# Kernel optimization log

Hardware: AMD Instinct MI355X
Metric: run time of the kernel (lower is better)

Reference implementation:

```python
import jax, jax.numpy as jnp
import numpy as np

N_NODES = 50000
N_EDGES = 300000
D = 256          # in_dim = out_dim (residual)
DE = 256         # edge relation dim
K = 2            # num_kgs
H = 4            # heads
L = 2            # layers
DH = D // H


def _routed_linear(x, W, b, idx):
    # x:[E,din], W:[K,din,dout], b:[K,dout], idx:[E] in [0,K)
    # Compute all K branches (K is tiny) then select per edge.
    outs = jnp.einsum('ed,kdo->keo', x, W) + b[:, None, :]
    return outs[idx, jnp.arange(idx.shape[0])]


def _layernorm(x, g, b):
    mu = jnp.mean(x, axis=-1, keepdims=True)
    var = jnp.mean(jnp.square(x - mu), axis=-1, keepdims=True)
    return (x - mu) * jax.lax.rsqrt(var + 1e-5) * g + b


def _mga_layer(h, src, dst, kg_src, kg_dst, beta, rel,
               ln_g, ln_b, Wt, bt, Wq, bq, Wk, bk):
    N = h.shape[0]
    E = src.shape[0]
    residual = h
    hn = _layernorm(h, ln_g, ln_b)
    x_j = hn[src]                       # [E,D] gathered source feats
    x_i = hn[dst]                       # [E,D] gathered target feats
    # per-edge KG-routed transfer of concatenated (x_j, relation emb)
    xj_t = jax.nn.gelu(_routed_linear(jnp.concatenate([x_j, rel], axis=1), Wt, bt, kg_src),
                       approximate=False)
    q = _routed_linear(x_i, Wq, bq, kg_dst).reshape(E, H, DH)
    k = _routed_linear(xj_t, Wk, bk, kg_src).reshape(E, H, DH)
    # per-edge multi-head dot product, scaled by edge_beta_r then 1/sqrt(dh)
    att = jnp.sum(q * k, axis=-1) * beta[:, None] / jnp.sqrt(jnp.asarray(DH, h.dtype))  # [E,H]
    # scatter-softmax over incoming edges of each target node
    m = jax.ops.segment_max(att, dst, num_segments=N)          # [N,H]
    e = jnp.exp(att - m[dst])
    denom = jax.ops.segment_sum(e, dst, num_segments=N)        # [N,H]
    a = e / (denom[dst] + 1e-16)                                # [E,H]
    msg = (a[:, :, None] * xj_t.reshape(E, H, DH)).reshape(E, D)
    aggr = jax.ops.segment_sum(msg, dst, num_segments=N)        # [N,D]
    return residual + jax.nn.gelu(aggr, approximate=False)


def setup_inputs() -> dict:
    key = jax.random.key(0)
    ks = jax.random.split(key, 10)
    x = jax.random.normal(ks[0], (N_NODES, D), dtype=jnp.float32)
    edge_index = jax.random.randint(ks[1], (2, N_EDGES), 0, N_NODES, dtype=jnp.int32)
    edge_kg_index = jax.random.randint(ks[2], (2, N_EDGES), 0, K, dtype=jnp.int32)
    edge_beta_r = jax.random.uniform(ks[3], (N_EDGES,), dtype=jnp.float32)
    edge_rel_emb = jax.random.normal(ks[4], (N_EDGES, DE), dtype=jnp.float32)
    return {
        'x': x,
        'edge_index': edge_index,
        'edge_kg_index': edge_kg_index,
        'edge_beta_r': edge_beta_r,
        'edge_rel_emb': edge_rel_emb,
        'ln_g': jnp.ones((L, D), jnp.float32),
        'ln_b': jnp.zeros((L, D), jnp.float32),
        'Wt': jax.random.normal(ks[5], (L, K, D + DE, D), jnp.float32) / np.sqrt(D + DE),
        'bt': jnp.zeros((L, K, D), jnp.float32),
        'Wq': jax.random.normal(ks[6], (L, K, D, D), jnp.float32) / np.sqrt(D),
        'bq': jnp.zeros((L, K, D), jnp.float32),
        'Wk': jax.random.normal(ks[7], (L, K, D, D), jnp.float32) / np.sqrt(D),
        'bk': jnp.zeros((L, K, D), jnp.float32),
    }


def reference(x, edge_index, edge_kg_index, edge_beta_r, edge_rel_emb,
              ln_g, ln_b, Wt, bt, Wq, bq, Wk, bk):
    src, dst = edge_index[0], edge_index[1]          # j (source), i (target)
    kg_src, kg_dst = edge_kg_index[0], edge_kg_index[1]
    h = x  # dropout is identity in eval mode
    for l in range(L):
        h = _mga_layer(h, src, dst, kg_src, kg_dst, edge_beta_r, edge_rel_emb,
                       ln_g[l], ln_b[l], Wt[l], bt[l], Wq[l], bq[l], Wk[l], bk[l])
    return h
```

## Files before the change

kernel.cpp:

```cpp
#include <hip/hip_runtime.h>
#include <hip/hip_bf16.h>

#define NN 50000
#define NE 300000
#define DD 256
#define NCHUNK 293

typedef __hip_bfloat16 bf16;
typedef __attribute__((ext_vector_type(8))) short bf16x8;
typedef __attribute__((ext_vector_type(4))) float f32x4;

__device__ __forceinline__ float bf2f(bf16 v) { return __bfloat162float(v); }
__device__ __forceinline__ unsigned short f2b(float v) {
    bf16 t = __float2bfloat16(v);
    return *reinterpret_cast<unsigned short*>(&t);
}
__device__ __forceinline__ float b2f_bits(unsigned short u) {
    return __uint_as_float(((unsigned)u) << 16);
}
__device__ __forceinline__ float gelu_f(float v) {
    return 0.5f * v * (1.f + erff(v * 0.70710678118654752f));
}
__device__ __forceinline__ void gl2lds16(const uint4* g, uint4* l) {
    __builtin_amdgcn_global_load_lds(
        (const __attribute__((address_space(1))) void*)g,
        (__attribute__((address_space(3))) void*)l, 16, 0, 0);
}

__global__ void part_count(const int* __restrict__ kg, int* __restrict__ bcnt) {
    int base = blockIdx.x * 1024;
    __shared__ int wc[4];
    int t = threadIdx.x, wave = t >> 6, lane = t & 63;
    int cnt = 0;
    #pragma unroll
    for (int s = 0; s < 4; ++s) {
        int j = base + s * 256 + t;
        int is0 = (j < NE && kg[j] == 0) ? 1 : 0;
        unsigned long long m = __ballot(is0);
        if (lane == 0) cnt += __popcll(m);
    }
    if (lane == 0) wc[wave] = cnt;
    __syncthreads();
    if (t == 0) bcnt[blockIdx.x] = wc[0] + wc[1] + wc[2] + wc[3];
}

__global__ void part_scan(const int* __restrict__ bcnt, int* __restrict__ bofs,
                          int* __restrict__ meta, int n) {
    if (threadIdx.x == 0 && blockIdx.x == 0) {
        int run = 0;
        for (int i = 0; i < n; ++i) { bofs[i] = run; run += bcnt[i]; }
        meta[0] = run;
    }
}

__global__ void part_scatter(const int* __restrict__ kg, const int* __restrict__ bofs,
                             const int* __restrict__ meta, int* __restrict__ perm) {
    int base = blockIdx.x * 1024;
    int c0 = meta[0];
    __shared__ int wz[4];
    int t = threadIdx.x, wave = t >> 6, lane = t & 63;
    int zrun = bofs[blockIdx.x];
    for (int s = 0; s < 4; ++s) {
        int j = base + s * 256 + t;
        int valid = j < NE;
        int is0 = (valid && kg[j] == 0) ? 1 : 0;
        unsigned long long m = __ballot(is0);
        int zb = __popcll(m & ((1ull << lane) - 1ull));
        if (lane == 0) wz[wave] = __popcll(m);
        __syncthreads();
        int wbefore = 0;
        for (int w = 0; w < wave; ++w) wbefore += wz[w];
        int zeros_before = zrun + wbefore + zb;
        if (valid) {
            int pos = is0 ? zeros_before : (c0 + (j - zeros_before));
            perm[pos] = j;
        }
        int stepz = wz[0] + wz[1] + wz[2] + wz[3];
        __syncthreads();
        zrun += stepz;
    }
}

__global__ void deg_hist(const int* __restrict__ dst, int* __restrict__ deg) {
    int i = blockIdx.x * blockDim.x + threadIdx.x;
    if (i < NE) atomicAdd(&deg[dst[i]], 1);
}

__global__ __launch_bounds__(1024) void scan_nodes(const int* __restrict__ deg,
                                                   int* __restrict__ ofs) {
    __shared__ int pex[1025];
    int t = threadIdx.x;
    const int C = (NN + 1023) / 1024;
    int base = t * C;
    int s = 0;
    for (int j = 0; j < C; ++j) { int idx = base + j; if (idx < NN) s += deg[idx]; }
    pex[t + 1] = s;
    __syncthreads();
    if (t == 0) {
        pex[0] = 0;
        for (int i = 1; i <= 1024; ++i) pex[i] += pex[i - 1];
    }
    __syncthreads();
    int run = pex[t];
    for (int j = 0; j < C; ++j) {
        int idx = base + j;
        if (idx < NN) { ofs[idx] = run; run += deg[idx]; }
    }
    if (t == 1023) ofs[NN] = pex[1024];
}

__global__ void copy_int(const int* __restrict__ a, int* __restrict__ b, int n) {
    int i = blockIdx.x * blockDim.x + threadIdx.x;
    if (i < n) b[i] = a[i];
}

__global__ void csr_fill(const int* __restrict__ dst, int* __restrict__ cur,
                         int* __restrict__ eid) {
    int i = blockIdx.x * blockDim.x + threadIdx.x;
    if (i < NE) {
        int p = atomicAdd(&cur[dst[i]], 1);
        eid[p] = i;
    }
}

__global__ void cast_x_kernel(const float* __restrict__ x, float* __restrict__ h, int n4) {
    for (int i = blockIdx.x * blockDim.x + threadIdx.x; i < n4; i += gridDim.x * blockDim.x)
        ((float4*)h)[i] = ((const float4*)x)[i];
}

__global__ void f2b_vec_kernel(const float* __restrict__ in, ushort* __restrict__ out, long n4) {
    long i0 = (long)blockIdx.x * blockDim.x + threadIdx.x;
    long stride = (long)gridDim.x * blockDim.x;
    for (long i = i0; i < n4; i += stride) {
        float4 v = ((const float4*)in)[i];
        ushort4 o;
        o.x = f2b(v.x); o.y = f2b(v.y); o.z = f2b(v.z); o.w = f2b(v.w);
        ((ushort4*)out)[i] = o;
    }
}

__global__ void transpose_w_kernel(const float* __restrict__ in, ushort* __restrict__ out,
                                   int shift, long total) {
    long i0 = (long)blockIdx.x * blockDim.x + threadIdx.x;
    long stride = (long)gridDim.x * blockDim.x;
    long dmask = ((long)1 << shift) - 1;
    for (long i = i0; i < total; i += stride) {
        long d = i & dmask;
        long rest = i >> shift;
        long o = rest & 255;
        long s = rest >> 8;
        out[i] = f2b(in[((s << shift) + d) * 256 + o]);
    }
}

__global__ void fill_kernel(float* __restrict__ p, float v, int n) {
    for (int i = blockIdx.x * blockDim.x + threadIdx.x; i < n; i += gridDim.x * blockDim.x)
        p[i] = v;
}

__global__ __launch_bounds__(256) void ln_kernel(const float* __restrict__ h,
        const float* __restrict__ g, const float* __restrict__ b, bf16* __restrict__ hn) {
    int n = blockIdx.x * 4 + (threadIdx.x >> 6);
    if (n >= NN) return;
    int t = threadIdx.x & 63;
    float4 v = ((const float4*)(h + (size_t)n * DD))[t];
    float s  = v.x + v.y + v.z + v.w;
    float s2 = v.x * v.x + v.y * v.y + v.z * v.z + v.w * v.w;
    #pragma unroll
    for (int off = 32; off; off >>= 1) {
        s  += __shfl_down(s, off);
        s2 += __shfl_down(s2, off);
    }
    s = __shfl(s, 0); s2 = __shfl(s2, 0);
    float mu  = s * (1.f / DD);
    float var = s2 * (1.f / DD) - mu * mu;
    float rs  = rsqrtf(var + 1e-5f);
    float vv[4] = {v.x, v.y, v.z, v.w};
    ushort4 pk;
    unsigned short* pku = (unsigned short*)&pk;
    #pragma unroll
    for (int j = 0; j < 4; ++j) {
        int c = t * 4 + j;
        pku[j] = f2b((vv[j] - mu) * rs * g[c] + b[c]);
    }
    ((ushort4*)(hn + (size_t)n * DD))[t] = pk;
}

__global__ __launch_bounds__(512) void qn_mfma(
        const bf16* __restrict__ hn, const ushort* __restrict__ WqT,
        const float* __restrict__ bq, ushort* __restrict__ qn) {
    __shared__ uint4 xh[64 * 32];
    __shared__ float bqs[2][256];
    int t = threadIdx.x;
    int n0 = blockIdx.x * 64;
    int wave = t >> 6, lane = t & 63;
    if (t < 256) { bqs[0][t] = bq[t]; bqs[1][t] = bq[256 + t]; }
    const uint4* hn4 = (const uint4*)hn;
    #pragma unroll
    for (int j = 0; j < 4; ++j) {
        int pr = wave * 4 + j;
        int r2 = pr * 2 + (lane >> 5);
        int node = n0 + r2; if (node >= NN) node = NN - 1;
        int s = lane & 31;
        gl2lds16(hn4 + (size_t)node * 32 + (s ^ (r2 & 7)), &xh[pr * 64]);
    }
    __syncthreads();
    int lr = lane & 15, lg = lane >> 4;
    f32x4 acc[2][2][4];
    #pragma unroll
    for (int b = 0; b < 2; ++b)
        #pragma unroll
        for (int m = 0; m < 2; ++m)
            #pragma unroll
            for (int n = 0; n < 4; ++n) acc[b][m][n] = (f32x4){0.f, 0.f, 0.f, 0.f};
    const char* xhb = (const char*)xh;
    const ushort* qr0 = WqT + (size_t)(wave * 32 + lr) * 256 + lg * 8;
    const ushort* qr1 = WqT + (size_t)(wave * 32 + 16 + lr) * 256 + lg * 8;
    #pragma unroll
    for (int kk = 0; kk < 8; ++kk) {
        bf16x8 a00 = *(const bf16x8*)(qr0 + kk * 32);
        bf16x8 a01 = *(const bf16x8*)(qr1 + kk * 32);
        bf16x8 a10 = *(const bf16x8*)(qr0 + 65536 + kk * 32);
        bf16x8 a11 = *(const bf16x8*)(qr1 + 65536 + kk * 32);
        bf16x8 bfr[4];
        #pragma unroll
        for (int n = 0; n < 4; ++n) {
            int r = n * 16 + lr;
            bfr[n] = *(const bf16x8*)(xhb + r * 512 + (((kk * 4 + lg) ^ (r & 7)) << 4));
        }
        #pragma unroll
        for (int n = 0; n < 4; ++n) {
            acc[0][0][n] = __builtin_amdgcn_mfma_f32_16x16x32_bf16(a00, bfr[n], acc[0][0][n], 0, 0, 0);
            acc[0][1][n] = __builtin_amdgcn_mfma_f32_16x16x32_bf16(a01, bfr[n], acc[0][1][n], 0, 0, 0);
            acc[1][0][n] = __builtin_amdgcn_mfma_f32_16x16x32_bf16(a10, bfr[n], acc[1][0][n], 0, 0, 0);
            acc[1][1][n] = __builtin_amdgcn_mfma_f32_16x16x32_bf16(a11, bfr[n], acc[1][1][n], 0, 0, 0);
        }
    }
    #pragma unroll
    for (int n = 0; n < 4; ++n) {
        int e = n * 16 + lr;
        int node = n0 + e;
        if (node < NN) {
            #pragma unroll
            for (int br = 0; br < 2; ++br)
                #pragma unroll
                for (int m = 0; m < 2; ++m) {
                    int ob = wave * 32 + m * 16 + lg * 4;
                    f32x4 a = acc[br][m][n];
                    ushort4 pk;
                    unsigned short* pu = (unsigned short*)&pk;
                    #pragma unroll
                    for (int r = 0; r < 4; ++r) pu[r] = f2b(a[r] + bqs[br][ob + r]);
                    *(ushort4*)(qn + ((size_t)br * NN + node) * 256 + ob) = pk;
                }
        }
    }
}

template<int RELB>
__global__ __launch_bounds__(512, 4) void transfer_mfma(
        const bf16* __restrict__ hn, const float* __restrict__ rel,
        const ushort* __restrict__ relb,
        const int* __restrict__ src, const int* __restrict__ dst,
        const int* __restrict__ kgd,
        const int* __restrict__ perm, const int* __restrict__ meta,
        const ushort* __restrict__ WtT, const float* __restrict__ bt,
        const ushort* __restrict__ WkT, const float* __restrict__ bk,
        const ushort* __restrict__ qn, const float* __restrict__ beta,
        bf16* __restrict__ xjt, float* __restrict__ att) {
    __shared__ uint4 xh[64 * 32];
    __shared__ float bts[256], bks[256];
    __shared__ float patt[8][64];
    __shared__ int sge[64], ssrc[64], sdst[64], sgd[64], sval[64];
    int t = threadIdx.x;
    int c0 = meta[0];
    int tiles0 = (c0 + 63) >> 6;
    int tiles1 = (NE - c0 + 63) >> 6;
    int bid = blockIdx.x;
    if (bid >= tiles0 + tiles1) return;
    int kgt, start, end;
    if (bid < tiles0) { kgt = 0; start = bid * 64; end = c0; }
    else              { kgt = 1; start = c0 + (bid - tiles0) * 64; end = NE; }
    int wave = t >> 6, lane = t & 63;
    if (t < 64) {
        int pos = start + t;
        int v = pos < end;
        int ge = perm[v ? pos : end - 1];
        sge[t] = ge; sval[t] = v; ssrc[t] = src[ge]; sdst[t] = dst[ge]; sgd[t] = kgd[ge];
    } else if (t >= 256) {
        int c = t & 255;
        bts[c] = bt[kgt * 256 + c];
        bks[c] = bk[kgt * 256 + c];
    }
    __syncthreads();
    const uint4* hn4 = (const uint4*)hn;
    #pragma unroll
    for (int j = 0; j < 4; ++j) {
        int pr = wave * 4 + j;
        int r2 = pr * 2 + (lane >> 5);
        int s = lane & 31;
        gl2lds16(hn4 + (size_t)ssrc[r2] * 32 + (s ^ (r2 & 7)), &xh[pr * 64]);
    }
    __syncthreads();
    int lr = lane & 15, lg = lane >> 4;
    f32x4 acc[2][4];
    #pragma unroll
    for (int m = 0; m < 2; ++m)
        #pragma unroll
        for (int n = 0; n < 4; ++n) acc[m][n] = (f32x4){0.f, 0.f, 0.f, 0.f};
    const char* xhb = (const char*)xh;
    const ushort* wb = WtT + (size_t)kgt * 131072;
    const ushort* wrow0 = wb + (size_t)(wave * 32 + lr) * 512 + lg * 8;
    const ushort* wrow1 = wb + (size_t)(wave * 32 + 16 + lr) * 512 + lg * 8;
    #pragma unroll
    for (int kk = 0; kk < 8; ++kk) {
        bf16x8 a0 = *(const bf16x8*)(wrow0 + kk * 32);
        bf16x8 a1 = *(const bf16x8*)(wrow1 + kk * 32);
        bf16x8 bfr[4];
        #pragma unroll
        for (int n = 0; n < 4; ++n) {
            int r = n * 16 + lr;
            bfr[n] = *(const bf16x8*)(xhb + r * 512 + (((kk * 4 + lg) ^ (r & 7)) << 4));
        }
        #pragma unroll
        for (int m = 0; m < 2; ++m)
            #pragma unroll
            for (int n = 0; n < 4; ++n)
                acc[m][n] = __builtin_amdgcn_mfma_f32_16x16x32_bf16((m ? a1 : a0), bfr[n], acc[m][n], 0, 0, 0);
    }
    __syncthreads();
    if (RELB) {
        const uint4* rb4 = (const uint4*)relb;
        #pragma unroll
        for (int j = 0; j < 4; ++j) {
            int pr = wave * 4 + j;
            int r2 = pr * 2 + (lane >> 5);
            int s = lane & 31;
            gl2lds16(rb4 + (size_t)sge[r2] * 32 + (s ^ (r2 & 7)), &xh[pr * 64]);
        }
    } else {
        #pragma unroll
        for (int i = 0; i < 8; ++i) {
            int r = i * 8 + wave;
            float4 f = ((const float4*)(rel + (size_t)sge[r] * 256))[lane];
            ushort4 o;
            o.x = f2b(f.x); o.y = f2b(f.y); o.z = f2b(f.z); o.w = f2b(f.w);
            int s = lane >> 1;
            char* bp = (char*)&xh[r * 32] + (((s ^ (r & 7)) << 4) | ((lane & 1) << 3));
            *(ushort4*)bp = o;
        }
    }
    __syncthreads();
    #pragma unroll
    for (int kk = 8; kk < 16; ++kk) {
        bf16x8 a0 = *(const bf16x8*)(wrow0 + kk * 32);
        bf16x8 a1 = *(const bf16x8*)(wrow1 + kk * 32);
        int ks = (kk & 7) * 4 + lg;
        bf16x8 bfr[4];
        #pragma unroll
        for (int n = 0; n < 4; ++n) {
            int r = n * 16 + lr;
            bfr[n] = *(const bf16x8*)(xhb + r * 512 + ((ks ^ (r & 7)) << 4));
        }
        #pragma unroll
        for (int m = 0; m < 2; ++m)
            #pragma unroll
            for (int n = 0; n < 4; ++n)
                acc[m][n] = __builtin_amdgcn_mfma_f32_16x16x32_bf16((m ? a1 : a0), bfr[n], acc[m][n], 0, 0, 0);
    }
    __syncthreads();
    char* xob = (char*)xh;
    #pragma unroll
    for (int n = 0; n < 4; ++n) {
        int e = n * 16 + lr;
        #pragma unroll
        for (int m = 0; m < 2; ++m) {
            int ob = wave * 32 + m * 16 + lg * 4;
            f32x4 a = acc[m][n];
            ushort4 pk;
            unsigned short* pu = (unsigned short*)&pk;
            #pragma unroll
            for (int r = 0; r < 4; ++r)
                pu[r] = f2b(gelu_f(a[r] + bts[ob + r]));
            int bofs = ob * 2;
            int slot = ((bofs >> 4) ^ (e & 7));
            *(ushort4*)(xob + e * 512 + slot * 16 + (bofs & 15)) = pk;
        }
    }
    __syncthreads();
    #pragma unroll
    for (int m = 0; m < 2; ++m)
        #pragma unroll
        for (int n = 0; n < 4; ++n) acc[m][n] = (f32x4){0.f, 0.f, 0.f, 0.f};
    const ushort* kbw = WkT + (size_t)kgt * 65536;
    const ushort* kr0 = kbw + (size_t)(wave * 32 + lr) * 256 + lg * 8;
    const ushort* kr1 = kbw + (size_t)(wave * 32 + 16 + lr) * 256 + lg * 8;
    #pragma unroll
    for (int kk = 0; kk < 8; ++kk) {
        bf16x8 a0 = *(const bf16x8*)(kr0 + kk * 32);
        bf16x8 a1 = *(const bf16x8*)(kr1 + kk * 32);
        bf16x8 bfr[4];
        #pragma unroll
        for (int n = 0; n < 4; ++n) {
            int r = n * 16 + lr;
            bfr[n] = *(const bf16x8*)(xob + r * 512 + (((kk * 4 + lg) ^ (r & 7)) << 4));
        }
        #pragma unroll
        for (int n = 0; n < 4; ++n) {
            acc[0][n] = __builtin_amdgcn_mfma_f32_16x16x32_bf16(a0, bfr[n], acc[0][n], 0, 0, 0);
            acc[1][n] = __builtin_amdgcn_mfma_f32_16x16x32_bf16(a1, bfr[n], acc[1][n], 0, 0, 0);
        }
    }
    float p[4];
    #pragma unroll
    for (int n = 0; n < 4; ++n) {
        int e = n * 16 + lr;
        size_t qb = ((size_t)sgd[e] * NN + sdst[e]) * 256;
        float s = 0.f;
        #pragma unroll
        for (int m = 0; m < 2; ++m) {
            int ob = wave * 32 + m * 16 + lg * 4;
            ushort4 qv = *(const ushort4*)(qn + qb + ob);
            f32x4 kcv = acc[m][n];
            s = fmaf(b2f_bits(qv.x), kcv[0] + bks[ob + 0], s);
            s = fmaf(b2f_bits(qv.y), kcv[1] + bks[ob + 1], s);
            s = fmaf(b2f_bits(qv.z), kcv[2] + bks[ob + 2], s);
            s = fmaf(b2f_bits(qv.w), kcv[3] + bks[ob + 3], s);
        }
        p[n] = s;
    }
    #pragma unroll
    for (int n = 0; n < 4; ++n) {
        p[n] += __shfl_xor(p[n], 16);
        p[n] += __shfl_xor(p[n], 32);
    }
    if (lane < 16) {
        #pragma unroll
        for (int n = 0; n < 4; ++n) patt[wave][n * 16 + lr] = p[n];
    }
    uint4* xjv = (uint4*)xjt;
    #pragma unroll
    for (int i = 0; i < 4; ++i) {
        int flat = i * 512 + t;
        int r = flat >> 5, c = flat & 31;
        if (sval[r])
            xjv[(size_t)sge[r] * 32 + c] = *(const uint4*)(xob + r * 512 + ((c ^ (r & 7)) << 4));
    }
    __syncthreads();
    if (t < 256) {
        int e = t & 63, h = t >> 6;
        if (sval[e]) {
            int ge = sge[e];
            att[(size_t)ge * 4 + h] = (patt[2 * h][e] + patt[2 * h + 1][e]) * beta[ge] * 0.125f;
        }
    }
}

__global__ __launch_bounds__(256) void aggregate_kernel(
        const float* __restrict__ att, const bf16* __restrict__ xjt,
        const int* __restrict__ eid, const int* __restrict__ ofs,
        float* __restrict__ h) {
    int node = blockIdx.x * 4 + (threadIdx.x >> 6);
    if (node >= NN) return;
    int lane = threadIdx.x & 63;
    int hh = lane >> 4;
    int beg = ofs[node], end = ofs[node + 1];
    float m = -1e30f;
    for (int i = beg; i < end; ++i)
        m = fmaxf(m, att[(size_t)eid[i] * 4 + hh]);
    float den = 0.f;
    float a0 = 0.f, a1 = 0.f, a2 = 0.f, a3 = 0.f;
    for (int i = beg; i < end; ++i) {
        int e = eid[i];
        float wgt = expf(att[(size_t)e * 4 + hh] - m);
        den += wgt;
        ushort4 v = *(const ushort4*)((const ushort*)xjt + (size_t)e * 256 + lane * 4);
        a0 = fmaf(wgt, b2f_bits(v.x), a0);
        a1 = fmaf(wgt, b2f_bits(v.y), a1);
        a2 = fmaf(wgt, b2f_bits(v.z), a2);
        a3 = fmaf(wgt, b2f_bits(v.w), a3);
    }
    float inv = 1.f / (den + 1e-16f);
    float4 hv = ((float4*)(h + (size_t)node * 256))[lane];
    hv.x += gelu_f(a0 * inv);
    hv.y += gelu_f(a1 * inv);
    hv.z += gelu_f(a2 * inv);
    hv.w += gelu_f(a3 * inv);
    ((float4*)(h + (size_t)node * 256))[lane] = hv;
}

extern "C" void kernel_launch(void* const* d_in, const int* in_sizes, int n_in,
                              void* d_out, int out_size, void* d_ws, size_t ws_size,
                              hipStream_t stream) {
    const float* x    = (const float*)d_in[0];
    const int*   ei   = (const int*)d_in[1];
    const int*   ekg  = (const int*)d_in[2];
    const float* beta = (const float*)d_in[3];
    const float* rel  = (const float*)d_in[4];
    const float* ln_g = (const float*)d_in[5];
    const float* ln_b = (const float*)d_in[6];
    const float* Wt   = (const float*)d_in[7];
    const float* bt   = (const float*)d_in[8];
    const float* Wq   = (const float*)d_in[9];
    const float* bq   = (const float*)d_in[10];
    const float* Wk   = (const float*)d_in[11];
    const float* bk   = (const float*)d_in[12];

    float* h = (float*)d_out;

    const int* srcp = ei;
    const int* dstp = ei + NE;
    const int* kgs  = ekg;
    const int* kgd  = ekg + NE;

    char* w = (char*)d_ws;
    float*  att   = (float*)w;  w += (size_t)NE * 4 * 4;
    bf16*   hn    = (bf16*)w;   w += (size_t)NN * DD * 2;
    bf16*   xjt   = (bf16*)w;   w += (size_t)NE * DD * 2;
    ushort* qn    = (ushort*)w; w += (size_t)2 * NN * DD * 2;
    ushort* WtT   = (ushort*)w; w += (size_t)4 * 256 * 512 * 2;
    ushort* WqT   = (ushort*)w; w += (size_t)4 * 256 * 256 * 2;
    ushort* WkT   = (ushort*)w; w += (size_t)4 * 256 * 256 * 2;
    int* perm_src = (int*)w;    w += (size_t)NE * 4;
    int* bcnt0    = (int*)w;    w += NCHUNK * 4;
    int* bofs0    = (int*)w;    w += NCHUNK * 4;
    int* meta0    = (int*)w;    w += 64;
    int* deg      = (int*)w;    w += (size_t)NN * 4;
    int* ofs      = (int*)w;    w += (size_t)(NN + 1) * 4;
    int* cur      = (int*)w;    w += (size_t)NN * 4;
    int* eid      = (int*)w;    w += (size_t)NE * 4;
    size_t used = (size_t)(w - (char*)d_ws);
    ushort* relb = (ushort*)w;
    int use_relb = (ws_size >= used + (size_t)NE * DD * 2) ? 1 : 0;

    part_count<<<NCHUNK, 256, 0, stream>>>(kgs, bcnt0);
    part_scan<<<1, 64, 0, stream>>>(bcnt0, bofs0, meta0, NCHUNK);
    part_scatter<<<NCHUNK, 256, 0, stream>>>(kgs, bofs0, meta0, perm_src);

    fill_kernel<<<64, 256, 0, stream>>>((float*)deg, 0.f, NN);
    deg_hist<<<(NE + 255) / 256, 256, 0, stream>>>(dstp, deg);
    scan_nodes<<<1, 1024, 0, stream>>>(deg, ofs);
    copy_int<<<(NN + 255) / 256, 256, 0, stream>>>(ofs, cur, NN);
    csr_fill<<<(NE + 255) / 256, 256, 0, stream>>>(dstp, cur, eid);

    cast_x_kernel<<<2048, 256, 0, stream>>>(x, h, NN * DD / 4);
    if (use_relb)
        f2b_vec_kernel<<<2048, 256, 0, stream>>>(rel, relb, (long)NE * DD / 4);
    transpose_w_kernel<<<512, 256, 0, stream>>>(Wt, WtT, 9, (long)4 * 256 * 512);
    transpose_w_kernel<<<256, 256, 0, stream>>>(Wq, WqT, 8, (long)4 * 256 * 256);
    transpose_w_kernel<<<256, 256, 0, stream>>>(Wk, WkT, 8, (long)4 * 256 * 256);

    const int EBP = (NE + 126) / 64;
    const int QB  = (NN + 63) / 64;
    const int AGB = (NN + 3) / 4;
    for (int l = 0; l < 2; ++l) {
        ln_kernel<<<AGB, 256, 0, stream>>>(h, ln_g + l * DD, ln_b + l * DD, hn);
        qn_mfma<<<QB, 512, 0, stream>>>(hn, WqT + (size_t)l * 2 * 256 * 256, bq + l * 512, qn);
        if (use_relb)
            transfer_mfma<1><<<EBP, 512, 0, stream>>>(hn, rel, relb, srcp, dstp, kgd,
                    perm_src, meta0,
                    WtT + (size_t)l * 2 * 256 * 512, bt + l * 512,
                    WkT + (size_t)l * 2 * 256 * 256, bk + l * 512, qn, beta, xjt, att);
        else
            transfer_mfma<0><<<EBP, 512, 0, stream>>>(hn, rel, relb, srcp, dstp, kgd,
                    perm_src, meta0,
                    WtT + (size_t)l * 2 * 256 * 512, bt + l * 512,
                    WkT + (size_t)l * 2 * 256 * 256, bk + l * 512, qn, beta, xjt, att);
        aggregate_kernel<<<AGB, 256, 0, stream>>>(att, xjt, eid, ofs, h);
    }
}
```

Baseline: 1.226 ms.

## Fuse layernorm into aggregate and input copy, prefetch q, use tanh GELU

Removes the separate cast and layernorm kernels. The input copy is folded into the first layernorm, and the layer-1 layernorm is computed inside the layer-0 aggregate kernel, which saves a full pass over h. The q values are prefetched before the MFMA loops, and s_setprio raises wave priority around the MFMA loops. The exact erf GELU is replaced with the tanh approximation and expf with __expf, which changes the numerics slightly compared with the reference's exact GELU.

```diff
diff --git a/kernel.cpp b/kernel.cpp
--- a/kernel.cpp
+++ b/kernel.cpp
@@ -19,7 +19,11 @@
     return __uint_as_float(((unsigned)u) << 16);
 }
 __device__ __forceinline__ float gelu_f(float v) {
-    return 0.5f * v * (1.f + erff(v * 0.70710678118654752f));
+    float v2 = v * v;
+    float z  = v * fmaf(v2, 0.044715f, 1.0f) * 0.7978845608f;
+    float e  = __expf(2.0f * z);
+    float th = 1.0f - 2.0f / (e + 1.0f);
+    return 0.5f * v * (1.0f + th);
 }
 __device__ __forceinline__ void gl2lds16(const uint4* g, uint4* l) {
     __builtin_amdgcn_global_load_lds(
@@ -123,11 +127,6 @@
     }
 }
 
-__global__ void cast_x_kernel(const float* __restrict__ x, float* __restrict__ h, int n4) {
-    for (int i = blockIdx.x * blockDim.x + threadIdx.x; i < n4; i += gridDim.x * blockDim.x)
-        ((float4*)h)[i] = ((const float4*)x)[i];
-}
-
 __global__ void f2b_vec_kernel(const float* __restrict__ in, ushort* __restrict__ out, long n4) {
     long i0 = (long)blockIdx.x * blockDim.x + threadIdx.x;
     long stride = (long)gridDim.x * blockDim.x;
@@ -158,12 +157,14 @@
         p[i] = v;
 }
 
-__global__ __launch_bounds__(256) void ln_kernel(const float* __restrict__ h,
-        const float* __restrict__ g, const float* __restrict__ b, bf16* __restrict__ hn) {
+__global__ __launch_bounds__(256) void lnx_kernel(const float* __restrict__ x,
+        const float* __restrict__ g, const float* __restrict__ b,
+        float* __restrict__ h, bf16* __restrict__ hn) {
     int n = blockIdx.x * 4 + (threadIdx.x >> 6);
     if (n >= NN) return;
     int t = threadIdx.x & 63;
-    float4 v = ((const float4*)(h + (size_t)n * DD))[t];
+    float4 v = ((const float4*)(x + (size_t)n * DD))[t];
+    ((float4*)(h + (size_t)n * DD))[t] = v;
     float s  = v.x + v.y + v.z + v.w;
     float s2 = v.x * v.x + v.y * v.y + v.z * v.z + v.w * v.w;
     #pragma unroll
@@ -303,6 +304,17 @@
     }
     __syncthreads();
     int lr = lane & 15, lg = lane >> 4;
+    ushort4 kv[2][4];
+    #pragma unroll
+    for (int n = 0; n < 4; ++n) {
+        int e = n * 16 + lr;
+        size_t qb = ((size_t)sgd[e] * NN + sdst[e]) * 256;
+        #pragma unroll
+        for (int m = 0; m < 2; ++m) {
+            int ob = wave * 32 + m * 16 + lg * 4;
+            kv[m][n] = *(const ushort4*)(qn + qb + ob);
+        }
+    }
     f32x4 acc[2][4];
     #pragma unroll
     for (int m = 0; m < 2; ++m)
@@ -312,6 +324,7 @@
     const ushort* wb = WtT + (size_t)kgt * 131072;
     const ushort* wrow0 = wb + (size_t)(wave * 32 + lr) * 512 + lg * 8;
     const ushort* wrow1 = wb + (size_t)(wave * 32 + 16 + lr) * 512 + lg * 8;
+    __builtin_amdgcn_s_setprio(1);
     #pragma unroll
     for (int kk = 0; kk < 8; ++kk) {
         bf16x8 a0 = *(const bf16x8*)(wrow0 + kk * 32);
@@ -328,6 +341,7 @@
             for (int n = 0; n < 4; ++n)
                 acc[m][n] = __builtin_amdgcn_mfma_f32_16x16x32_bf16((m ? a1 : a0), bfr[n], acc[m][n], 0, 0, 0);
     }
+    __builtin_amdgcn_s_setprio(0);
     __syncthreads();
     if (RELB) {
         const uint4* rb4 = (const uint4*)relb;
@@ -351,6 +365,7 @@
         }
     }
     __syncthreads();
+    __builtin_amdgcn_s_setprio(1);
     #pragma unroll
     for (int kk = 8; kk < 16; ++kk) {
         bf16x8 a0 = *(const bf16x8*)(wrow0 + kk * 32);
@@ -368,6 +383,7 @@
             for (int n = 0; n < 4; ++n)
                 acc[m][n] = __builtin_amdgcn_mfma_f32_16x16x32_bf16((m ? a1 : a0), bfr[n], acc[m][n], 0, 0, 0);
     }
+    __builtin_amdgcn_s_setprio(0);
     __syncthreads();
     char* xob = (char*)xh;
     #pragma unroll
@@ -395,6 +411,7 @@
     const ushort* kbw = WkT + (size_t)kgt * 65536;
     const ushort* kr0 = kbw + (size_t)(wave * 32 + lr) * 256 + lg * 8;
     const ushort* kr1 = kbw + (size_t)(wave * 32 + 16 + lr) * 256 + lg * 8;
+    __builtin_amdgcn_s_setprio(1);
     #pragma unroll
     for (int kk = 0; kk < 8; ++kk) {
         bf16x8 a0 = *(const bf16x8*)(kr0 + kk * 32);
@@ -411,16 +428,15 @@
             acc[1][n] = __builtin_amdgcn_mfma_f32_16x16x32_bf16(a1, bfr[n], acc[1][n], 0, 0, 0);
         }
     }
+    __builtin_amdgcn_s_setprio(0);
     float p[4];
     #pragma unroll
     for (int n = 0; n < 4; ++n) {
-        int e = n * 16 + lr;
-        size_t qb = ((size_t)sgd[e] * NN + sdst[e]) * 256;
         float s = 0.f;
         #pragma unroll
         for (int m = 0; m < 2; ++m) {
             int ob = wave * 32 + m * 16 + lg * 4;
-            ushort4 qv = *(const ushort4*)(qn + qb + ob);
+            ushort4 qv = kv[m][n];
             f32x4 kcv = acc[m][n];
             s = fmaf(b2f_bits(qv.x), kcv[0] + bks[ob + 0], s);
             s = fmaf(b2f_bits(qv.y), kcv[1] + bks[ob + 1], s);
@@ -456,10 +472,12 @@
     }
 }
 
+template<int WRITE_HN>
 __global__ __launch_bounds__(256) void aggregate_kernel(
         const float* __restrict__ att, const bf16* __restrict__ xjt,
         const int* __restrict__ eid, const int* __restrict__ ofs,
-        float* __restrict__ h) {
+        float* __restrict__ h, const float* __restrict__ g, const float* __restrict__ b,
+        bf16* __restrict__ hn) {
     int node = blockIdx.x * 4 + (threadIdx.x >> 6);
     if (node >= NN) return;
     int lane = threadIdx.x & 63;
@@ -472,7 +490,7 @@
     float a0 = 0.f, a1 = 0.f, a2 = 0.f, a3 = 0.f;
     for (int i = beg; i < end; ++i) {
         int e = eid[i];
-        float wgt = expf(att[(size_t)e * 4 + hh] - m);
+        float wgt = __expf(att[(size_t)e * 4 + hh] - m);
         den += wgt;
         ushort4 v = *(const ushort4*)((const ushort*)xjt + (size_t)e * 256 + lane * 4);
         a0 = fmaf(wgt, b2f_bits(v.x), a0);
@@ -487,6 +505,28 @@
     hv.z += gelu_f(a2 * inv);
     hv.w += gelu_f(a3 * inv);
     ((float4*)(h + (size_t)node * 256))[lane] = hv;
+    if (WRITE_HN) {
+        float s  = hv.x + hv.y + hv.z + hv.w;
+        float s2 = hv.x * hv.x + hv.y * hv.y + hv.z * hv.z + hv.w * hv.w;
+        #pragma unroll
+        for (int off = 32; off; off >>= 1) {
+            s  += __shfl_down(s, off);
+            s2 += __shfl_down(s2, off);
+        }
+        s = __shfl(s, 0); s2 = __shfl(s2, 0);
+        float mu  = s * (1.f / DD);
+        float var = s2 * (1.f / DD) - mu * mu;
+        float rs  = rsqrtf(var + 1e-5f);
+        float vv[4] = {hv.x, hv.y, hv.z, hv.w};
+        ushort4 pk;
+        unsigned short* pku = (unsigned short*)&pk;
+        #pragma unroll
+        for (int j = 0; j < 4; ++j) {
+            int c = lane * 4 + j;
+            pku[j] = f2b((vv[j] - mu) * rs * g[c] + b[c]);
+        }
+        ((ushort4*)(hn + (size_t)node * DD))[lane] = pk;
+    }
 }
 
 extern "C" void kernel_launch(void* const* d_in, const int* in_sizes, int n_in,
@@ -543,7 +583,6 @@
     copy_int<<<(NN + 255) / 256, 256, 0, stream>>>(ofs, cur, NN);
     csr_fill<<<(NE + 255) / 256, 256, 0, stream>>>(dstp, cur, eid);
 
-    cast_x_kernel<<<2048, 256, 0, stream>>>(x, h, NN * DD / 4);
     if (use_relb)
         f2b_vec_kernel<<<2048, 256, 0, stream>>>(rel, relb, (long)NE * DD / 4);
     transpose_w_kernel<<<512, 256, 0, stream>>>(Wt, WtT, 9, (long)4 * 256 * 512);
@@ -553,8 +592,9 @@
     const int EBP = (NE + 126) / 64;
     const int QB  = (NN + 63) / 64;
     const int AGB = (NN + 3) / 4;
+
+    lnx_kernel<<<AGB, 256, 0, stream>>>(x, ln_g, ln_b, h, hn);
     for (int l = 0; l < 2; ++l) {
-        ln_kernel<<<AGB, 256, 0, stream>>>(h, ln_g + l * DD, ln_b + l * DD, hn);
         qn_mfma<<<QB, 512, 0, stream>>>(hn, WqT + (size_t)l * 2 * 256 * 256, bq + l * 512, qn);
         if (use_relb)
             transfer_mfma<1><<<EBP, 512, 0, stream>>>(hn, rel, relb, srcp, dstp, kgd,
@@ -566,6 +606,11 @@
                     perm_src, meta0,
                     WtT + (size_t)l * 2 * 256 * 512, bt + l * 512,
                     WkT + (size_t)l * 2 * 256 * 256, bk + l * 512, qn, beta, xjt, att);
-        aggregate_kernel<<<AGB, 256, 0, stream>>>(att, xjt, eid, ofs, h);
-    }
-}
+        if (l == 0)
+            aggregate_kernel<1><<<AGB, 256, 0, stream>>>(att, xjt, eid, ofs, h,
+                    ln_g + DD, ln_b + DD, hn);
+        else
+            aggregate_kernel<0><<<AGB, 256, 0, stream>>>(att, xjt, eid, ofs, h,
+                    ln_g, ln_b, hn);
+    }
+}
```

New measurement: 1.206 ms. Within noise of the previous version (-1.6%).
